# Kernel tuning notes

Hardware: AMD Instinct MI355X
Metric: run time of the kernel (lower is better)

The kernel has to match this reference:

```python
import jax, jax.numpy as jnp
import numpy as np

B, S, D = 4, 2048, 1024
H = 16
HD = D // H  # 64


def setup_inputs() -> dict:
    key = jax.random.key(0)
    ks = jax.random.split(key, 6)
    scale = 1.0 / np.sqrt(D)
    return {
        "x": jax.random.normal(ks[0], (B, S, D), dtype=jnp.float32),
        "W_q": jax.random.normal(ks[1], (D, D), dtype=jnp.float32) * scale,
        "W_k": jax.random.normal(ks[2], (D, D), dtype=jnp.float32) * scale,
        "W_v": jax.random.normal(ks[3], (D, D), dtype=jnp.float32) * scale,
        "W_o": jax.random.normal(ks[4], (D, D), dtype=jnp.float32) * scale,
        "b_o": jax.random.normal(ks[5], (D,), dtype=jnp.float32) * 0.01,
    }


def reference(x, W_q, W_k, W_v, W_o, b_o):
    b, n, _ = x.shape
    # projections (Linear stores weight as [out,in]; here W_* are [in,out])
    q = (x @ W_q).reshape(b, n, H, HD).transpose(0, 2, 1, 3)  # [b,h,n,hd]
    k = (x @ W_k).reshape(b, n, H, HD).transpose(0, 2, 1, 3)
    v = (x @ W_v).reshape(b, n, H, HD).transpose(0, 2, 1, 3)
    scores = jnp.einsum("bhqd,bhkd->bhqk", q, k) / np.sqrt(HD).astype(np.float32)
    causal = jnp.tril(jnp.ones((n, n), dtype=bool))  # True = keep
    scores = jnp.where(causal, scores, -jnp.inf)
    weights = jax.nn.softmax(scores, axis=-1)
    ctx = jnp.einsum("bhqk,bhkd->bhqd", weights, v)
    ctx = ctx.transpose(0, 2, 1, 3).reshape(b, n, D)
    return ctx @ W_o + b_o
```

## Files before the change

kernel.cpp:

```cpp
#include <hip/hip_runtime.h>
#include <cstdint>

#define S_LEN 2048
#define D_MODEL 1024
#define NH 16
#define HDIM 64
#define BATCH 4

typedef __attribute__((ext_vector_type(8))) __bf16 bfrag;
typedef __attribute__((ext_vector_type(4))) float ffrag;

__device__ __forceinline__ unsigned short f2bf(float f) {
    union { float f; uint32_t u; } v; v.f = f;
    uint32_t u = v.u;
    u += 0x7fff + ((u >> 16) & 1);
    return (unsigned short)(u >> 16);
}

__device__ __forceinline__ bfrag ld_frag(const unsigned short* p) {
    union { uint4 u; bfrag b; } x;
    x.u = *(const uint4*)p;
    return x.b;
}

__device__ __forceinline__ float fast_exp2(float x) {
#if __has_builtin(__builtin_amdgcn_exp2f)
    return __builtin_amdgcn_exp2f(x);
#else
    return __expf(x * 0.6931471805599453f);
#endif
}

__device__ __forceinline__ uint32_t pack_bf16(float a, float b) {
    union { float f; uint32_t u; } x, y; x.f = a; y.f = b;
    return __builtin_amdgcn_perm(y.u + 0x8000u, x.u + 0x8000u, 0x07060302u);
}

__device__ __forceinline__ void g2l16(const unsigned short* g, unsigned short* l) {
    __builtin_amdgcn_global_load_lds(
        (const __attribute__((address_space(1))) void*)g,
        (__attribute__((address_space(3))) void*)l, 16, 0, 0);
}

__global__ __launch_bounds__(256) void prep_kernel(const float* __restrict__ x,
                                                   const float* __restrict__ w0,
                                                   const float* __restrict__ w1,
                                                   const float* __restrict__ w2,
                                                   const float* __restrict__ w3,
                                                   unsigned short* __restrict__ xb,
                                                   unsigned short* __restrict__ wt) {
    __shared__ float tile[32][33];
    int bid = blockIdx.x;
    int t = threadIdx.x;
    if (bid < 4096) {
        int i = bid * 256 + t;
        const float4* p = (const float4*)x + (size_t)i * 2;
        float4 a = p[0], b = p[1];
        union { unsigned short u[8]; uint4 v; } o;
        o.u[0]=f2bf(a.x); o.u[1]=f2bf(a.y); o.u[2]=f2bf(a.z); o.u[3]=f2bf(a.w);
        o.u[4]=f2bf(b.x); o.u[5]=f2bf(b.y); o.u[6]=f2bf(b.z); o.u[7]=f2bf(b.w);
        ((uint4*)xb)[i] = o.v;
    } else {
        int r = bid - 4096;
        int mat = r >> 10;
        int rem = r & 1023;
        const float* w = (mat == 0) ? w0 : (mat == 1) ? w1 : (mat == 2) ? w2 : w3;
        int n0 = (rem & 31) * 32, k0 = (rem >> 5) * 32;
        int tx = t & 31, ty = t >> 5;
        for (int i = 0; i < 32; i += 8)
            tile[ty + i][tx] = w[(size_t)(k0 + ty + i) * D_MODEL + n0 + tx];
        __syncthreads();
        unsigned short* o = wt + (size_t)mat * D_MODEL * D_MODEL;
        for (int i = 0; i < 32; i += 8)
            o[(size_t)(n0 + ty + i) * D_MODEL + (k0 + tx)] = f2bf(tile[tx][ty + i]);
    }
}

__global__ __launch_bounds__(256) void transpose_v_kernel(const unsigned short* __restrict__ Vb,
                                                          unsigned short* __restrict__ Vtb) {
    __shared__ unsigned short tile[64][72];
    int st = blockIdx.x;
    int bh = blockIdx.y;
    int t = threadIdx.x;
    int sl = t >> 2, dc = (t & 3) * 16;
    const unsigned short* src = Vb + ((size_t)bh * S_LEN + st * 64 + sl) * HDIM + dc;
    *(uint4*)&tile[sl][dc]     = *(const uint4*)(src);
    *(uint4*)&tile[sl][dc + 8] = *(const uint4*)(src + 8);
    __syncthreads();
    int d = t >> 2, sc = (t & 3) * 16;
    union { unsigned short u[16]; uint4 v[2]; } o;
#pragma unroll
    for (int i = 0; i < 16; i++) o.u[i] = tile[sc + i][d];
    unsigned short* dst = Vtb + ((size_t)bh * HDIM + d) * S_LEN + st * 64 + sc;
    *(uint4*)(dst)     = o.v[0];
    *(uint4*)(dst + 8) = o.v[1];
}

#define GBUF 4096
#define NKT  (D_MODEL / 32)

__global__ __launch_bounds__(256) void gemm_kernel(
    const unsigned short* __restrict__ A,
    const unsigned short* __restrict__ Bt,
    int mode,
    unsigned short* __restrict__ Qb,
    unsigned short* __restrict__ Kb,
    unsigned short* __restrict__ Vb,
    float* __restrict__ Out,
    const float* __restrict__ bias) {
    __shared__ unsigned short As[3 * GBUF];
    __shared__ unsigned short Bs[3 * GBUF];
    int t = threadIdx.x;

    int nwg  = (int)(gridDim.x * gridDim.y);
    int flat = (int)(blockIdx.y * gridDim.x + blockIdx.x);
    int cpx  = nwg >> 3;
    int wid  = (flat & 7) * cpx + (flat >> 3);
    int m0 = (wid / (int)gridDim.x) * 128;
    int n0 = (wid % (int)gridDim.x) * 128;

    int wave = t >> 6, lane = t & 63;
    int quad = lane >> 4, lrow = lane & 15;
    int wm = (wave & 1) * 64, wn = (wave >> 1) * 64;

    ffrag acc[4][4];
    const ffrag fz = {0.f, 0.f, 0.f, 0.f};
    for (int i = 0; i < 4; i++)
        for (int j = 0; j < 4; j++) acc[i][j] = fz;

    int c0 = t, c1 = 256 + t;
    int r0 = c0 >> 2, cg0 = (c0 & 3) ^ ((r0 >> 1) & 3);
    int r1 = c1 >> 2, cg1 = (c1 & 3) ^ ((r1 >> 1) & 3);
    const unsigned short* A0 = A + (size_t)(m0 + r0) * D_MODEL + cg0 * 8;
    const unsigned short* A1 = A + (size_t)(m0 + r1) * D_MODEL + cg1 * 8;
    const unsigned short* B0 = Bt + (size_t)(n0 + r0) * D_MODEL + cg0 * 8;
    const unsigned short* B1 = Bt + (size_t)(n0 + r1) * D_MODEL + cg1 * 8;
    unsigned short* lA0 = &As[(wave * 64) * 8];
    unsigned short* lA1 = &As[(256 + wave * 64) * 8];
    unsigned short* lB0 = &Bs[(wave * 64) * 8];
    unsigned short* lB1 = &Bs[(256 + wave * 64) * 8];

    g2l16(A0, lA0);
    g2l16(A1, lA1);
    g2l16(B0, lB0);
    g2l16(B1, lB1);
    g2l16(A0 + 32, lA0 + GBUF);
    g2l16(A1 + 32, lA1 + GBUF);
    g2l16(B0 + 32, lB0 + GBUF);
    g2l16(B1 + 32, lB1 + GBUF);

    int bufA = 0, bufB = GBUF, bufC = 2 * GBUF;

    for (int kt = 0; kt < NKT - 1; ++kt) {
        asm volatile("s_waitcnt vmcnt(4)\n\ts_barrier" ::: "memory");
        __builtin_amdgcn_sched_barrier(0);
        if (kt + 2 < NKT) {
            int ko = (kt + 2) * 32;
            g2l16(A0 + ko, lA0 + bufC);
            g2l16(A1 + ko, lA1 + bufC);
            g2l16(B0 + ko, lB0 + bufC);
            g2l16(B1 + ko, lB1 + bufC);
        }
        bfrag af[4], bf[4];
        for (int mi = 0; mi < 4; mi++) {
            int row = wm + mi * 16 + lrow;
            af[mi] = ld_frag(&As[bufA + row * 32 + ((quad ^ ((row >> 1) & 3)) * 8)]);
        }
        for (int ni = 0; ni < 4; ni++) {
            int row = wn + ni * 16 + lrow;
            bf[ni] = ld_frag(&Bs[bufA + row * 32 + ((quad ^ ((row >> 1) & 3)) * 8)]);
        }
        for (int mi = 0; mi < 4; mi++)
            for (int ni = 0; ni < 4; ni++)
                acc[mi][ni] = __builtin_amdgcn_mfma_f32_16x16x32_bf16(af[mi], bf[ni], acc[mi][ni], 0, 0, 0);
        int tmp = bufA; bufA = bufB; bufB = bufC; bufC = tmp;
    }
    asm volatile("s_waitcnt vmcnt(0)\n\ts_barrier" ::: "memory");
    __builtin_amdgcn_sched_barrier(0);
    {
        bfrag af[4], bf[4];
        for (int mi = 0; mi < 4; mi++) {
            int row = wm + mi * 16 + lrow;
            af[mi] = ld_frag(&As[bufA + row * 32 + ((quad ^ ((row >> 1) & 3)) * 8)]);
        }
        for (int ni = 0; ni < 4; ni++) {
            int row = wn + ni * 16 + lrow;
            bf[ni] = ld_frag(&Bs[bufA + row * 32 + ((quad ^ ((row >> 1) & 3)) * 8)]);
        }
        for (int mi = 0; mi < 4; mi++)
            for (int ni = 0; ni < 4; ni++)
                acc[mi][ni] = __builtin_amdgcn_mfma_f32_16x16x32_bf16(af[mi], bf[ni], acc[mi][ni], 0, 0, 0);
    }

    for (int mi = 0; mi < 4; mi++) {
        int row = m0 + wm + mi * 16 + quad * 4;
        for (int ni = 0; ni < 4; ni++) {
            int col = n0 + wn + ni * 16 + lrow;
            for (int r = 0; r < 4; r++) {
                float v = acc[mi][ni][r];
                int m = row + r;
                if (mode == 0) {
                    int matid = col >> 10;
                    int nn = col & 1023;
                    int h = nn >> 6, d = nn & 63;
                    int b = m >> 11, s = m & 2047;
                    size_t bh = (size_t)(b * NH + h);
                    if (matid == 0)      Qb[(bh * S_LEN + s) * HDIM + d] = f2bf(v);
                    else if (matid == 1) Kb[(bh * S_LEN + s) * HDIM + d] = f2bf(v);
                    else                 Vb[(bh * S_LEN + s) * HDIM + d] = f2bf(v);
                } else {
                    Out[(size_t)m * D_MODEL + col] = v + bias[col];
                }
            }
        }
    }
}

#define SCALE2 0.18033688f
#define CSHIFT 4.0f
#define KVBUF 4096

__global__ __launch_bounds__(256, 4) void attn_kernel(
    const unsigned short* __restrict__ Qb,
    const unsigned short* __restrict__ Kb,
    const unsigned short* __restrict__ Vtb,
    unsigned short* __restrict__ ctxb) {
    __shared__ unsigned short Ks[2 * KVBUF];
    __shared__ unsigned short Vs[2 * KVBUF];
    __shared__ unsigned short Ps[4 * 16 * 64];
    int flat = (int)(blockIdx.y * gridDim.x + blockIdx.x);
    int wid  = (flat & 7) * 128 + (flat >> 3);
    int bx = wid & 15;
    int bh = wid >> 4;
    int t = threadIdx.x;
    int wave = t >> 6, lane = t & 63;
    int quad = lane >> 4, lrow = lane & 15;
    int swz = lrow & 7;
    int ca = (quad ^ swz) * 8;
    int cb = ca ^ 32;

    union { uint4 u; bfrag b; } one_u;
    one_u.u.x = 0x3F803F80u; one_u.u.y = 0x3F803F80u;
    one_u.u.z = 0x3F803F80u; one_u.u.w = 0x3F803F80u;
    bfrag onef = one_u.b;

    const unsigned short* Qg = Qb + (size_t)bh * S_LEN * HDIM;
    const unsigned short* Kg = Kb + (size_t)bh * S_LEN * HDIM;
    const unsigned short* Vg = Vtb + (size_t)bh * HDIM * S_LEN;
    int b = bh >> 4, h = bh & 15;

    int c0 = t, c1 = 256 + t;
    int kr0 = c0 >> 3, kp0 = (c0 & 7) ^ (kr0 & 7);
    int kr1 = c1 >> 3, kp1 = (c1 & 7) ^ (kr1 & 7);
    const unsigned short* pK0 = Kg + (size_t)kr0 * HDIM + kp0 * 8;
    const unsigned short* pK1 = Kg + (size_t)kr1 * HDIM + kp1 * 8;
    const unsigned short* pV0 = Vg + (size_t)kr0 * S_LEN + kp0 * 8;
    const unsigned short* pV1 = Vg + (size_t)kr1 * S_LEN + kp1 * 8;
    unsigned short* lK0 = &Ks[(wave * 64) * 8];
    unsigned short* lK1 = &Ks[(256 + wave * 64) * 8];
    unsigned short* lV0 = &Vs[(wave * 64) * 8];
    unsigned short* lV1 = &Vs[(256 + wave * 64) * 8];
    unsigned short* Pw = &Ps[wave * 16 * 64];

    for (int ph = 0; ph < 2; ph++) {
        int qc = ph == 0 ? (31 - bx) : bx;
        int qw = qc * 64 + wave * 16;
        int nk = qc + 1;

        bfrag qf[2];
#pragma unroll
        for (int c = 0; c < 2; c++)
            qf[c] = ld_frag(Qg + (size_t)(qw + lrow) * HDIM + c * 32 + quad * 8);

        ffrag acc[4];
        ffrag acc_l;
        const ffrag fz = {0.f, 0.f, 0.f, 0.f};
#pragma unroll
        for (int d = 0; d < 4; d++) acc[d] = fz;
        acc_l = fz;

        __syncthreads();
        g2l16(pK0, lK0);
        g2l16(pK1, lK1);
        g2l16(pV0, lV0);
        g2l16(pV1, lV1);

        for (int kt = 0; kt < nk; kt++) {
            int kbase = kt * 64;
            int buf = (kt & 1) * KVBUF;
            __syncthreads();
            if (kt + 1 < nk) {
                int nb = ((kt + 1) & 1) * KVBUF;
                size_t krow_off = (size_t)(kbase + 64) * HDIM;
                g2l16(pK0 + krow_off, lK0 + nb);
                g2l16(pK1 + krow_off, lK1 + nb);
                g2l16(pV0 + kbase + 64, lV0 + nb);
                g2l16(pV1 + kbase + 64, lV1 + nb);
            }

            ffrag sf[4];
#pragma unroll
            for (int ki = 0; ki < 4; ki++) {
                int krow = buf + (ki * 16 + lrow) * 64;
                bfrag ka = ld_frag(&Ks[krow + ca]);
                bfrag kb = ld_frag(&Ks[krow + cb]);
                ffrag s = fz;
                s = __builtin_amdgcn_mfma_f32_16x16x32_bf16(ka, qf[0], s, 0, 0, 0);
                s = __builtin_amdgcn_mfma_f32_16x16x32_bf16(kb, qf[1], s, 0, 0, 0);
                sf[ki] = s;
            }

            int qg = qw + lrow;
            bool need_mask = (kt == nk - 1);
            float sv[16];
#pragma unroll
            for (int ki = 0; ki < 4; ki++)
#pragma unroll
                for (int r = 0; r < 4; r++) {
                    float v = sf[ki][r];
                    if (need_mask) {
                        int key = kbase + ki * 16 + quad * 4 + r;
                        v = (key <= qg) ? v : -3.0e38f;
                    }
                    sv[ki * 4 + r] = fast_exp2(__builtin_fmaf(v, SCALE2, -CSHIFT));
                }
            int prow = lrow * 64;
#pragma unroll
            for (int ki = 0; ki < 4; ki++) {
                uint2 w2;
                w2.x = pack_bf16(sv[ki * 4 + 0], sv[ki * 4 + 1]);
                w2.y = pack_bf16(sv[ki * 4 + 2], sv[ki * 4 + 3]);
                int pc = ((ki * 2 + (quad >> 1)) ^ swz) * 8 + (quad & 1) * 4;
                *(uint2*)&Pw[prow + pc] = w2;
            }

            bfrag pf0 = ld_frag(&Pw[prow + ca]);
            bfrag pf1 = ld_frag(&Pw[prow + cb]);
            acc_l = __builtin_amdgcn_mfma_f32_16x16x32_bf16(onef, pf0, acc_l, 0, 0, 0);
            acc_l = __builtin_amdgcn_mfma_f32_16x16x32_bf16(onef, pf1, acc_l, 0, 0, 0);
#pragma unroll
            for (int di = 0; di < 4; di++) {
                int vrow = buf + (di * 16 + lrow) * 64;
                bfrag va = ld_frag(&Vs[vrow + ca]);
                bfrag vb = ld_frag(&Vs[vrow + cb]);
                acc[di] = __builtin_amdgcn_mfma_f32_16x16x32_bf16(va, pf0, acc[di], 0, 0, 0);
                acc[di] = __builtin_amdgcn_mfma_f32_16x16x32_bf16(vb, pf1, acc[di], 0, 0, 0);
            }
        }

        float rl = __builtin_amdgcn_rcpf(acc_l[0]);
#pragma unroll
        for (int di = 0; di < 4; di++) {
            uint2 w2;
            w2.x = pack_bf16(acc[di][0] * rl, acc[di][1] * rl);
            w2.y = pack_bf16(acc[di][2] * rl, acc[di][3] * rl);
            *(uint2*)&Pw[lrow * 64 + di * 16 + quad * 4] = w2;
        }
        int ql = lane >> 3, cc = lane & 7;
#pragma unroll
        for (int p = 0; p < 2; p++) {
            uint4 vv = *(uint4*)&Pw[(p * 8 + ql) * 64 + cc * 8];
            int q = qw + p * 8 + ql;
            *(uint4*)(ctxb + ((size_t)b * S_LEN + q) * D_MODEL + h * HDIM + cc * 8) = vv;
        }
    }
}

extern "C" void kernel_launch(void* const* d_in, const int* in_sizes, int n_in,
                              void* d_out, int out_size, void* d_ws, size_t ws_size,
                              hipStream_t stream) {
    const float* x   = (const float*)d_in[0];
    const float* W_q = (const float*)d_in[1];
    const float* W_k = (const float*)d_in[2];
    const float* W_v = (const float*)d_in[3];
    const float* W_o = (const float*)d_in[4];
    const float* b_o = (const float*)d_in[5];
    float* out = (float*)d_out;

    unsigned short* xb   = (unsigned short*)d_ws;
    unsigned short* Wt   = xb + (size_t)8192 * 1024;
    unsigned short* Qb   = Wt + (size_t)4 * 1024 * 1024;
    unsigned short* Kb   = Qb + (size_t)64 * 2048 * 64;
    unsigned short* Vtb  = Kb + (size_t)64 * 2048 * 64;
    unsigned short* ctxb = Vtb + (size_t)64 * 2048 * 64;
    unsigned short* Vb   = ctxb;
    unsigned short* Wto  = Wt + (size_t)3 * 1024 * 1024;

    prep_kernel<<<8192, 256, 0, stream>>>(x, W_q, W_k, W_v, W_o, xb, Wt);
    gemm_kernel<<<dim3(24, 64), 256, 0, stream>>>(xb, Wt, 0, Qb, Kb, Vb, nullptr, nullptr);
    transpose_v_kernel<<<dim3(32, 64), 256, 0, stream>>>(Vb, Vtb);
    attn_kernel<<<dim3(16, 64), 256, 0, stream>>>(Qb, Kb, Vtb, ctxb);
    gemm_kernel<<<dim3(8, 64), 256, 0, stream>>>(ctxb, Wto, 1, nullptr, nullptr, nullptr, out, b_o);
}
```

Before: 281.1 us.

## Use 256x256-tile 512-thread GEMM with 4-stage pipeline for QKV projection

Replaces the 128x128 QKV projection GEMM with a dedicated 256x256-tile kernel using 8 waves, a 4-deep LDS ring buffer, and MFMA phases split into two halves with setprio raised around the MFMA bursts. Larger tiles raise arithmetic intensity and cut global reloads of A and B. The output projection GEMM gets its own specialized kernel without the mode branch. The cost is more LDS (128KB per block) and more accumulator registers, which lowers occupancy, and only 384 blocks are launched.

```diff
diff --git a/kernel.cpp b/kernel.cpp
--- a/kernel.cpp
+++ b/kernel.cpp
@@ -96,16 +96,160 @@
     *(uint4*)(dst + 8) = o.v[1];
 }
 
-#define GBUF 4096
+#define MFMA_BF16 __builtin_amdgcn_mfma_f32_16x16x32_bf16
+
+#define QBUF 8192
 #define NKT  (D_MODEL / 32)
 
-__global__ __launch_bounds__(256) void gemm_kernel(
+#define Q_TILE(bufA)                                                              \
+  do {                                                                            \
+    bfrag bf_[4], af_[4];                                                         \
+    _Pragma("unroll")                                                             \
+    for (int ni = 0; ni < 4; ni++) {                                              \
+      int row = wc + ni * 16 + lrow;                                              \
+      bf_[ni] = ld_frag(&Bs[(bufA) + row * 32 + ((quad ^ ((row >> 1) & 3)) * 8)]);\
+    }                                                                             \
+    _Pragma("unroll")                                                             \
+    for (int mi = 0; mi < 4; mi++) {                                              \
+      int row = wr + mi * 16 + lrow;                                              \
+      af_[mi] = ld_frag(&As[(bufA) + row * 32 + ((quad ^ ((row >> 1) & 3)) * 8)]);\
+    }                                                                             \
+    asm volatile("s_waitcnt lgkmcnt(0)" ::: "memory");                            \
+    __builtin_amdgcn_sched_barrier(0);                                            \
+    __builtin_amdgcn_s_setprio(1);                                                \
+    _Pragma("unroll")                                                             \
+    for (int mi = 0; mi < 4; mi++)                                                \
+      _Pragma("unroll")                                                           \
+      for (int ni = 0; ni < 4; ni++)                                              \
+        acc[mi][ni] = MFMA_BF16(af_[mi], bf_[ni], acc[mi][ni], 0, 0, 0);          \
+    __builtin_amdgcn_s_setprio(0);                                                \
+    __builtin_amdgcn_sched_barrier(0);                                            \
+    _Pragma("unroll")                                                             \
+    for (int mi = 0; mi < 4; mi++) {                                              \
+      int row = wr + (mi + 4) * 16 + lrow;                                        \
+      af_[mi] = ld_frag(&As[(bufA) + row * 32 + ((quad ^ ((row >> 1) & 3)) * 8)]);\
+    }                                                                             \
+    asm volatile("s_waitcnt lgkmcnt(0)" ::: "memory");                            \
+    __builtin_amdgcn_sched_barrier(0);                                            \
+    __builtin_amdgcn_s_setprio(1);                                                \
+    _Pragma("unroll")                                                             \
+    for (int mi = 0; mi < 4; mi++)                                                \
+      _Pragma("unroll")                                                           \
+      for (int ni = 0; ni < 4; ni++)                                              \
+        acc[mi + 4][ni] = MFMA_BF16(af_[mi], bf_[ni], acc[mi + 4][ni], 0, 0, 0);  \
+    __builtin_amdgcn_s_setprio(0);                                                \
+  } while (0)
+
+__global__ __launch_bounds__(512, 2) void gemm256_kernel(
     const unsigned short* __restrict__ A,
     const unsigned short* __restrict__ Bt,
-    int mode,
     unsigned short* __restrict__ Qb,
     unsigned short* __restrict__ Kb,
-    unsigned short* __restrict__ Vb,
+    unsigned short* __restrict__ Vb) {
+    __shared__ unsigned short As[4 * QBUF];
+    __shared__ unsigned short Bs[4 * QBUF];
+    int t = threadIdx.x;
+
+    int gx   = (int)gridDim.x;
+    int nwg  = gx * (int)gridDim.y;
+    int flat = (int)(blockIdx.y * gridDim.x + blockIdx.x);
+    int cpx  = nwg >> 3;
+    int wid  = (flat & 7) * cpx + (flat >> 3);
+    int m0 = (wid / gx) * 256;
+    int n0 = (wid % gx) * 256;
+
+    int wave = t >> 6, lane = t & 63;
+    int quad = lane >> 4, lrow = lane & 15;
+    int wr = (wave & 1) * 128;
+    int wc = (wave >> 1) * 64;
+
+    ffrag acc[8][4];
+    const ffrag fz = {0.f, 0.f, 0.f, 0.f};
+#pragma unroll
+    for (int i = 0; i < 8; i++)
+#pragma unroll
+        for (int j = 0; j < 4; j++) acc[i][j] = fz;
+
+    int c0 = t, c1 = 512 + t;
+    int r0 = c0 >> 2, g0 = (c0 & 3) ^ ((r0 >> 1) & 3);
+    int r1 = c1 >> 2, g1 = (c1 & 3) ^ ((r1 >> 1) & 3);
+    const unsigned short* A0 = A + (size_t)(m0 + r0) * D_MODEL + g0 * 8;
+    const unsigned short* A1 = A + (size_t)(m0 + r1) * D_MODEL + g1 * 8;
+    const unsigned short* B0 = Bt + (size_t)(n0 + r0) * D_MODEL + g0 * 8;
+    const unsigned short* B1 = Bt + (size_t)(n0 + r1) * D_MODEL + g1 * 8;
+    unsigned short* lA0 = &As[(wave * 64) * 8];
+    unsigned short* lA1 = &As[(512 + wave * 64) * 8];
+    unsigned short* lB0 = &Bs[(wave * 64) * 8];
+    unsigned short* lB1 = &Bs[(512 + wave * 64) * 8];
+
+    g2l16(A0, lA0);
+    g2l16(A1, lA1);
+    g2l16(B0, lB0);
+    g2l16(B1, lB1);
+    g2l16(A0 + 32, lA0 + QBUF);
+    g2l16(A1 + 32, lA1 + QBUF);
+    g2l16(B0 + 32, lB0 + QBUF);
+    g2l16(B1 + 32, lB1 + QBUF);
+    g2l16(A0 + 64, lA0 + 2 * QBUF);
+    g2l16(A1 + 64, lA1 + 2 * QBUF);
+    g2l16(B0 + 64, lB0 + 2 * QBUF);
+    g2l16(B1 + 64, lB1 + 2 * QBUF);
+
+    for (int kt = 0; kt < NKT - 2; ++kt) {
+        asm volatile("s_waitcnt vmcnt(8)\n\ts_barrier" ::: "memory");
+        __builtin_amdgcn_sched_barrier(0);
+        if (kt < NKT - 3) {
+            int ko = (kt + 3) * 32;
+            int nb = ((kt + 3) & 3) * QBUF;
+            g2l16(A0 + ko, lA0 + nb);
+            g2l16(A1 + ko, lA1 + nb);
+            g2l16(B0 + ko, lB0 + nb);
+            g2l16(B1 + ko, lB1 + nb);
+        }
+        int bufA = (kt & 3) * QBUF;
+        Q_TILE(bufA);
+    }
+    {
+        asm volatile("s_waitcnt vmcnt(4)\n\ts_barrier" ::: "memory");
+        __builtin_amdgcn_sched_barrier(0);
+        int bufA = ((NKT - 2) & 3) * QBUF;
+        Q_TILE(bufA);
+    }
+    {
+        asm volatile("s_waitcnt vmcnt(0)\n\ts_barrier" ::: "memory");
+        __builtin_amdgcn_sched_barrier(0);
+        int bufA = ((NKT - 1) & 3) * QBUF;
+        Q_TILE(bufA);
+    }
+
+#pragma unroll
+    for (int mi = 0; mi < 8; mi++) {
+        int row = m0 + wr + mi * 16 + quad * 4;
+#pragma unroll
+        for (int ni = 0; ni < 4; ni++) {
+            int col = n0 + wc + ni * 16 + lrow;
+#pragma unroll
+            for (int r = 0; r < 4; r++) {
+                float v = acc[mi][ni][r];
+                int m = row + r;
+                int matid = col >> 10;
+                int nn = col & 1023;
+                int h = nn >> 6, d = nn & 63;
+                int b = m >> 11, s = m & 2047;
+                size_t bh = (size_t)(b * NH + h);
+                if (matid == 0)      Qb[(bh * S_LEN + s) * HDIM + d] = f2bf(v);
+                else if (matid == 1) Kb[(bh * S_LEN + s) * HDIM + d] = f2bf(v);
+                else                 Vb[(bh * S_LEN + s) * HDIM + d] = f2bf(v);
+            }
+        }
+    }
+}
+
+#define GBUF 4096
+
+__global__ __launch_bounds__(256) void gemm128_kernel(
+    const unsigned short* __restrict__ A,
+    const unsigned short* __restrict__ Bt,
     float* __restrict__ Out,
     const float* __restrict__ bias) {
     __shared__ unsigned short As[3 * GBUF];
@@ -172,7 +316,7 @@
         }
         for (int mi = 0; mi < 4; mi++)
             for (int ni = 0; ni < 4; ni++)
-                acc[mi][ni] = __builtin_amdgcn_mfma_f32_16x16x32_bf16(af[mi], bf[ni], acc[mi][ni], 0, 0, 0);
+                acc[mi][ni] = MFMA_BF16(af[mi], bf[ni], acc[mi][ni], 0, 0, 0);
         int tmp = bufA; bufA = bufB; bufB = bufC; bufC = tmp;
     }
     asm volatile("s_waitcnt vmcnt(0)\n\ts_barrier" ::: "memory");
@@ -189,28 +333,19 @@
         }
         for (int mi = 0; mi < 4; mi++)
             for (int ni = 0; ni < 4; ni++)
-                acc[mi][ni] = __builtin_amdgcn_mfma_f32_16x16x32_bf16(af[mi], bf[ni], acc[mi][ni], 0, 0, 0);
-    }
-
+                acc[mi][ni] = MFMA_BF16(af[mi], bf[ni], acc[mi][ni], 0, 0, 0);
+    }
+
+#pragma unroll
     for (int mi = 0; mi < 4; mi++) {
         int row = m0 + wm + mi * 16 + quad * 4;
+#pragma unroll
         for (int ni = 0; ni < 4; ni++) {
             int col = n0 + wn + ni * 16 + lrow;
+#pragma unroll
             for (int r = 0; r < 4; r++) {
-                float v = acc[mi][ni][r];
                 int m = row + r;
-                if (mode == 0) {
-                    int matid = col >> 10;
-                    int nn = col & 1023;
-                    int h = nn >> 6, d = nn & 63;
-                    int b = m >> 11, s = m & 2047;
-                    size_t bh = (size_t)(b * NH + h);
-                    if (matid == 0)      Qb[(bh * S_LEN + s) * HDIM + d] = f2bf(v);
-                    else if (matid == 1) Kb[(bh * S_LEN + s) * HDIM + d] = f2bf(v);
-                    else                 Vb[(bh * S_LEN + s) * HDIM + d] = f2bf(v);
-                } else {
-                    Out[(size_t)m * D_MODEL + col] = v + bias[col];
-                }
+                Out[(size_t)m * D_MODEL + col] = acc[mi][ni][r] + bias[col];
             }
         }
     }
@@ -387,8 +522,8 @@
     unsigned short* Wto  = Wt + (size_t)3 * 1024 * 1024;
 
     prep_kernel<<<8192, 256, 0, stream>>>(x, W_q, W_k, W_v, W_o, xb, Wt);
-    gemm_kernel<<<dim3(24, 64), 256, 0, stream>>>(xb, Wt, 0, Qb, Kb, Vb, nullptr, nullptr);
+    gemm256_kernel<<<dim3(12, 32), 512, 0, stream>>>(xb, Wt, Qb, Kb, Vb);
     transpose_v_kernel<<<dim3(32, 64), 256, 0, stream>>>(Vb, Vtb);
     attn_kernel<<<dim3(16, 64), 256, 0, stream>>>(Qb, Kb, Vtb, ctxb);
-    gemm_kernel<<<dim3(8, 64), 256, 0, stream>>>(ctxb, Wto, 1, nullptr, nullptr, nullptr, out, b_o);
-}
+    gemm128_kernel<<<dim3(8, 64), 256, 0, stream>>>(ctxb, Wto, out, b_o);
+}
```

Result: faster. 271.5 us (-3.4%).
